# Performance work log

Measured on AMD Instinct MI355X. Metric: run time of the kernel, lower is better.

The kernel has to match this reference:

```python
import jax, jax.numpy as jnp
import numpy as np

# Mamba2 defaults (mamba_ssm): expand=2, headdim=64, d_conv=4, ngroups=1
D_MODEL, D_STATE, D_INNER, HEADDIM, D_CONV = 512, 64, 1024, 64, 4
NHEADS = D_INNER // HEADDIM  # 16
CONV_DIM = D_INNER + 2 * D_STATE  # 1152
D_IN_PROJ = 2 * D_INNER + 2 * D_STATE + NHEADS  # 2192
BATCH, SEQLEN = 2, 2048
RMS_EPS = 1.1920929e-07  # torch nn.RMSNorm eps=None -> fp32 machine eps
GNORM_EPS = 1e-5  # mamba_ssm RMSNormGated default


def _rms(t, w, eps):
    return t * jax.lax.rsqrt(jnp.mean(t * t, axis=-1, keepdims=True) + eps) * w


def _mamba2(u, in_w, conv_w, conv_b, dt_bias, A_log, Dp, gnorm_w, out_w):
    """Mamba2 block forward (ngroups=1). u: (b, l, d_model) -> (b, l, d_model)."""
    b, l, _ = u.shape
    zxbcdt = jnp.einsum('bld,ed->ble', u, in_w)  # (b, l, 2192)
    z = zxbcdt[..., :D_INNER]
    xBC = zxbcdt[..., D_INNER:D_INNER + CONV_DIM]
    dt = jax.nn.softplus(zxbcdt[..., -NHEADS:] + dt_bias)  # (b, l, h)
    # causal depthwise conv, kernel D_CONV, then SiLU
    xp = jnp.pad(xBC, ((0, 0), (D_CONV - 1, 0), (0, 0)))
    xBC = conv_b + sum(xp[:, i:i + l, :] * conv_w[:, i] for i in range(D_CONV))
    xBC = jax.nn.silu(xBC)
    x = xBC[..., :D_INNER].reshape(b, l, NHEADS, HEADDIM)
    Bm = xBC[..., D_INNER:D_INNER + D_STATE]  # (b, l, n)
    Cm = xBC[..., D_INNER + D_STATE:]         # (b, l, n)
    dA = jnp.exp(dt * (-jnp.exp(A_log)))      # (b, l, h), decay per head

    def step(h, inp):
        dA_t, dt_t, B_t, C_t, x_t = inp  # (b,h) (b,h) (b,n) (b,n) (b,h,p)
        h = h * dA_t[:, :, None, None] + jnp.einsum('bh,bhp,bn->bhpn', dt_t, x_t, B_t)
        y = jnp.einsum('bhpn,bn->bhp', h, C_t)
        return h, y

    h0 = jnp.zeros((b, NHEADS, HEADDIM, D_STATE), u.dtype)
    xs = (jnp.swapaxes(dA, 0, 1), jnp.swapaxes(dt, 0, 1), jnp.swapaxes(Bm, 0, 1),
          jnp.swapaxes(Cm, 0, 1), jnp.swapaxes(x, 0, 1))
    _, ys = jax.lax.scan(step, h0, xs)  # (l, b, h, p)
    y = jnp.swapaxes(ys, 0, 1) + x * Dp[None, None, :, None]
    y = y.reshape(b, l, D_INNER)
    # gated RMSNorm: norm(y * silu(z)) * weight
    y = y * jax.nn.silu(z)
    y = _rms(y, gnorm_w, GNORM_EPS)
    return jnp.einsum('bli,oi->blo', y, out_w)


def _layer(x, pos_emb, pixel_mask, norm_ssm_w, norm_ffn_w, ffn_w1, ffn_b1, ffn_w2, ffn_b2,
           f_in_w, f_conv_w, f_conv_b, f_dt_bias, f_A_log, f_D, f_gnorm_w, f_out_w,
           b_in_w, b_conv_w, b_conv_b, b_dt_bias, b_A_log, b_D, b_gnorm_w, b_out_w):
    si = _rms(x, norm_ssm_w, RMS_EPS) + pos_emb
    fwd = _mamba2(si, f_in_w, f_conv_w, f_conv_b, f_dt_bias, f_A_log, f_D, f_gnorm_w, f_out_w)
    bwd = jnp.flip(_mamba2(jnp.flip(si, 1), b_in_w, b_conv_w, b_conv_b, b_dt_bias,
                           b_A_log, b_D, b_gnorm_w, b_out_w), 1)
    ssm_out = (fwd + bwd) * pixel_mask[..., None]  # merge='add'
    x = x + ssm_out
    h = _rms(x, norm_ffn_w, RMS_EPS)
    h = jax.nn.gelu(h @ ffn_w1.T + ffn_b1, approximate=False)
    return x + (h @ ffn_w2.T + ffn_b2)


def setup_inputs() -> dict:
    key = jax.random.key(0)
    ks = jax.random.split(key, 16)
    f32 = jnp.float32
    inp = {}
    inp['x'] = jax.random.normal(ks[0], (BATCH, SEQLEN, D_MODEL), f32)
    inp['pos_emb'] = jax.random.normal(ks[1], (BATCH, SEQLEN, D_MODEL), f32) * 0.02
    inp['pixel_mask'] = jnp.ones((BATCH, SEQLEN), f32)
    inp['norm_ssm_w'] = jnp.ones((D_MODEL,), f32)
    inp['norm_ffn_w'] = jnp.ones((D_MODEL,), f32)
    d_ffn = 4 * D_MODEL
    inp['ffn_w1'] = jax.random.normal(ks[2], (d_ffn, D_MODEL), f32) * 0.02
    inp['ffn_b1'] = jnp.zeros((d_ffn,), f32)
    inp['ffn_w2'] = jax.random.normal(ks[3], (D_MODEL, d_ffn), f32) * 0.02
    inp['ffn_b2'] = jnp.zeros((D_MODEL,), f32)
    i = 4
    for pre in ('f', 'b'):
        inp[pre + '_in_w'] = jax.random.normal(ks[i], (D_IN_PROJ, D_MODEL), f32) * 0.02; i += 1
        inp[pre + '_conv_w'] = jax.random.uniform(ks[i], (CONV_DIM, D_CONV), f32, -0.5, 0.5); i += 1
        inp[pre + '_conv_b'] = jnp.zeros((CONV_DIM,), f32)
        dt0 = jnp.exp(jax.random.uniform(ks[i], (NHEADS,), f32) * (jnp.log(0.1) - jnp.log(0.001)) + jnp.log(0.001)); i += 1
        inp[pre + '_dt_bias'] = dt0 + jnp.log(-jnp.expm1(-dt0))  # inverse softplus
        inp[pre + '_A_log'] = jnp.log(jax.random.uniform(ks[i], (NHEADS,), f32, 1.0, 16.0)); i += 1
        inp[pre + '_D'] = jnp.ones((NHEADS,), f32)
        inp[pre + '_gnorm_w'] = jnp.ones((D_INNER,), f32)
        inp[pre + '_out_w'] = jax.random.normal(ks[i], (D_MODEL, D_INNER), f32) * 0.02; i += 1
    return inp


def reference(x, pos_emb, pixel_mask, norm_ssm_w, norm_ffn_w, ffn_w1, ffn_b1, ffn_w2, ffn_b2,
              f_in_w, f_conv_w, f_conv_b, f_dt_bias, f_A_log, f_D, f_gnorm_w, f_out_w,
              b_in_w, b_conv_w, b_conv_b, b_dt_bias, b_A_log, b_D, b_gnorm_w, b_out_w):
    return _layer(x, pos_emb, pixel_mask, norm_ssm_w, norm_ffn_w, ffn_w1, ffn_b1, ffn_w2, ffn_b2,
                  f_in_w, f_conv_w, f_conv_b, f_dt_bias, f_A_log, f_D, f_gnorm_w, f_out_w,
                  b_in_w, b_conv_w, b_conv_b, b_dt_bias, b_A_log, b_D, b_gnorm_w, b_out_w)
```

## Files before the change

kernel.cpp:

```cpp
#include <hip/hip_runtime.h>
#include <hip/hip_bf16.h>

typedef unsigned short u16;
typedef unsigned int u32;
typedef __bf16 bf16x8 __attribute__((ext_vector_type(8)));
typedef float f32x4 __attribute__((ext_vector_type(4)));

typedef __attribute__((address_space(1))) void gvoid_t;
typedef __attribute__((address_space(3))) void lvoid_t;
__device__ __forceinline__ void lds_cp16(void* lds, const void* g) {
    __builtin_amdgcn_global_load_lds((gvoid_t*)g, (lvoid_t*)lds, 16, 0, 0);
}

__device__ __forceinline__ float bf2f(u16 v) {
    u32 x = (u32)v << 16;
    return __builtin_bit_cast(float, x);
}
__device__ __forceinline__ u16 f2bf(float f) {
    return __builtin_bit_cast(u16, (__bf16)f);
}

__device__ __forceinline__ float wave_sum(float v) {
    #pragma unroll
    for (int o = 32; o > 0; o >>= 1) v += __shfl_xor(v, o);
    return v;
}

__device__ __forceinline__ void cvt4(const float* __restrict__ s, u16* __restrict__ d) {
    float4 v = *(const float4*)s;
    ushort4 o;
    o.x = f2bf(v.x); o.y = f2bf(v.y); o.z = f2bf(v.z); o.w = f2bf(v.w);
    *(ushort4*)d = o;
}

__global__ __launch_bounds__(256) void k_prep(
    const float* __restrict__ f_inw, const float* __restrict__ b_inw,
    const float* __restrict__ f_ow, const float* __restrict__ b_ow,
    const float* __restrict__ w1, const float* __restrict__ w2,
    u16* __restrict__ INWF, u16* __restrict__ INWB,
    u16* __restrict__ OWF, u16* __restrict__ OWB,
    u16* __restrict__ W1B, u16* __restrict__ W2B,
    const float* __restrict__ x, const float* __restrict__ pe,
    const float* __restrict__ wrms, u16* __restrict__ sib) {
    if (blockIdx.x < 5376) {
        int g = blockIdx.x * 256 + threadIdx.x;
        if (g < 294912) {
            int i = g * 4, n = i >> 9;
            if (n < 2192) cvt4(f_inw + i, INWF + i);
            else *(ushort4*)(INWF + i) = make_ushort4(0, 0, 0, 0);
            return;
        }
        g -= 294912;
        if (g < 294912) {
            int i = g * 4, n = i >> 9;
            if (n < 2192) cvt4(b_inw + i, INWB + i);
            else *(ushort4*)(INWB + i) = make_ushort4(0, 0, 0, 0);
            return;
        }
        g -= 294912;
        if (g < 131072) { cvt4(f_ow + g * 4, OWF + g * 4); return; }
        g -= 131072;
        if (g < 131072) { cvt4(b_ow + g * 4, OWB + g * 4); return; }
        g -= 131072;
        if (g < 262144) { cvt4(w1 + g * 4, W1B + g * 4); return; }
        g -= 262144;
        cvt4(w2 + g * 4, W2B + g * 4);
        return;
    }
    int row = (blockIdx.x - 5376) * 4 + (threadIdx.x >> 6);
    int lane = threadIdx.x & 63;
    size_t base = (size_t)row * 512 + lane * 4;
    float4 xa = *(const float4*)(x + base);
    float4 xb = *(const float4*)(x + base + 256);
    float ss = xa.x * xa.x + xa.y * xa.y + xa.z * xa.z + xa.w * xa.w
             + xb.x * xb.x + xb.y * xb.y + xb.z * xb.z + xb.w * xb.w;
    ss = wave_sum(ss);
    float sc = rsqrtf(ss * (1.f / 512.f) + 1.1920929e-07f);
    float4 pa = *(const float4*)(pe + base);
    float4 pb = *(const float4*)(pe + base + 256);
    float4 wa = *(const float4*)(wrms + lane * 4);
    float4 wb = *(const float4*)(wrms + lane * 4 + 256);
    ushort4 oa, obv;
    oa.x = f2bf(xa.x * sc * wa.x + pa.x);
    oa.y = f2bf(xa.y * sc * wa.y + pa.y);
    oa.z = f2bf(xa.z * sc * wa.z + pa.z);
    oa.w = f2bf(xa.w * sc * wa.w + pa.w);
    obv.x = f2bf(xb.x * sc * wb.x + pb.x);
    obv.y = f2bf(xb.y * sc * wb.y + pb.y);
    obv.z = f2bf(xb.z * sc * wb.z + pb.z);
    obv.w = f2bf(xb.w * sc * wb.w + pb.w);
    *(ushort4*)(sib + base) = oa;
    *(ushort4*)(sib + base + 256) = obv;
}

__global__ __launch_bounds__(256) void k_gemm_in(
    const u16* __restrict__ A, const u16* __restrict__ W0, const u16* __restrict__ W1,
    u16* __restrict__ Z0, u16* __restrict__ Z1,
    u16* __restrict__ XB0, u16* __restrict__ XB1) {
    const int z = blockIdx.z;
    const u16* W = z ? W1 : W0;
    u16* Z = z ? Z1 : Z0;
    u16* XB = z ? XB1 : XB0;
    const int K = 512;

    __shared__ __align__(16) u16 SMEM[24576];
    u16* As = SMEM;
    u16* Bs = SMEM + 12288;

    const int t = threadIdx.x;
    const int lane = t & 63;
    const int w = t >> 6;
    const int m0 = blockIdx.y * 128;
    const int n0 = blockIdx.x * 128;
    const int wm = (w >> 1) * 64;
    const int wn = (w & 1) * 64;
    const int fr = lane & 15;
    const int ksw = (((lane >> 4) ^ ((fr >> 1) & 3)) & 3) * 8;

    f32x4 acc[4][4];
    #pragma unroll
    for (int i = 0; i < 4; ++i)
        #pragma unroll
        for (int j = 0; j < 4; ++j) acc[i][j] = (f32x4){0.f, 0.f, 0.f, 0.f};

    auto STAGE = [&](int buf, int kt) {
        #pragma unroll
        for (int j = 0; j < 2; ++j) {
            int off16 = j * 256 + t;
            int row = off16 >> 2;
            int kc = (((off16 & 3) ^ ((row >> 1) & 3)) & 3) * 8;
            int gm = m0 + row;
            if (z) gm = (gm & ~2047) | (2047 - (gm & 2047));
            lds_cp16(As + buf * 4096 + off16 * 8, A + (size_t)gm * K + kt + kc);
            lds_cp16(Bs + buf * 4096 + off16 * 8, W + (size_t)(n0 + row) * K + kt + kc);
        }
    };

    const int NS = 16;
    STAGE(0, 0);
    STAGE(1, 32);
    asm volatile("s_waitcnt vmcnt(4)" ::: "memory");
    __builtin_amdgcn_s_barrier();
    __builtin_amdgcn_sched_barrier(0);
    int b0 = 0, b1 = 1, b2 = 2;
    for (int i = 0; i < NS; ++i) {
        if (i + 2 < NS) STAGE(b2, (i + 2) << 5);
        const u16* Ac = As + b0 * 4096;
        const u16* Bc = Bs + b0 * 4096;
        bf16x8 af[4], bfr[4];
        #pragma unroll
        for (int ii = 0; ii < 4; ++ii) af[ii] = *(const bf16x8*)(Ac + (wm + ii * 16 + fr) * 32 + ksw);
        #pragma unroll
        for (int ii = 0; ii < 4; ++ii) bfr[ii] = *(const bf16x8*)(Bc + (wn + ii * 16 + fr) * 32 + ksw);
        #pragma unroll
        for (int ii = 0; ii < 4; ++ii)
            #pragma unroll
            for (int jj = 0; jj < 4; ++jj)
                acc[ii][jj] = __builtin_amdgcn_mfma_f32_16x16x32_bf16(af[ii], bfr[jj], acc[ii][jj], 0, 0, 0);
        if (i + 1 < NS) {
            if (i + 2 < NS) asm volatile("s_waitcnt vmcnt(4) lgkmcnt(0)" ::: "memory");
            else            asm volatile("s_waitcnt vmcnt(0) lgkmcnt(0)" ::: "memory");
            __builtin_amdgcn_s_barrier();
            __builtin_amdgcn_sched_barrier(0);
        }
        int bt = b0; b0 = b1; b1 = b2; b2 = bt;
    }
    __syncthreads();
    const int PAD = 136;
    #pragma unroll
    for (int i = 0; i < 4; ++i) {
        int rloc = wm + i * 16 + (lane >> 4) * 4;
        #pragma unroll
        for (int j = 0; j < 4; ++j) {
            int cloc = wn + j * 16 + fr;
            #pragma unroll
            for (int r = 0; r < 4; ++r)
                SMEM[(rloc + r) * PAD + cloc] = f2bf(acc[i][j][r]);
        }
    }
    __syncthreads();
    if (n0 < 1024) {
        #pragma unroll
        for (int it = 0; it < 4; ++it) {
            int row = it * 32 + w * 8 + (lane >> 3);
            #pragma unroll
            for (int half = 0; half < 2; ++half) {
                int col = half * 64 + (lane & 7) * 8;
                uint4 v = *(const uint4*)(SMEM + row * PAD + col);
                *(uint4*)(Z + (size_t)(m0 + row) * 1024 + n0 + col) = v;
            }
        }
    } else {
        #pragma unroll
        for (int it = 0; it < 4; ++it) {
            int row = it * 32 + w * 8 + (lane >> 3);
            #pragma unroll
            for (int half = 0; half < 2; ++half) {
                int col = half * 64 + (lane & 7) * 8;
                int cx = n0 - 1024 + col;
                if (cx < 1168) {
                    uint4 v = *(const uint4*)(SMEM + row * PAD + col);
                    *(uint4*)(XB + (size_t)(m0 + row) * 1184 + cx) = v;
                }
            }
        }
    }
}

template <int EPI>
__global__ __launch_bounds__(256) void k_gemm128(
    const u16* __restrict__ A0, const u16* __restrict__ A1,
    const u16* __restrict__ W0, const u16* __restrict__ W1,
    u16* __restrict__ C0, u16* __restrict__ C1, int N, int K,
    const float* __restrict__ bias, const float* __restrict__ resid,
    float* __restrict__ outf) {
    const int z = blockIdx.z;
    const u16* A = z ? A1 : A0;
    const u16* W = z ? W1 : W0;
    u16* C = z ? C1 : C0;

    __shared__ __align__(16) u16 SMEM[24576];
    u16* As = SMEM;
    u16* Bs = SMEM + 12288;

    const int t = threadIdx.x;
    const int lane = t & 63;
    const int w = t >> 6;
    const int m0 = blockIdx.y * 128;
    const int n0 = blockIdx.x * 128;
    const int wm = (w >> 1) * 64;
    const int wn = (w & 1) * 64;
    const int fr = lane & 15;
    const int ksw = (((lane >> 4) ^ ((fr >> 1) & 3)) & 3) * 8;

    f32x4 acc[4][4];
    #pragma unroll
    for (int i = 0; i < 4; ++i)
        #pragma unroll
        for (int j = 0; j < 4; ++j) acc[i][j] = (f32x4){0.f, 0.f, 0.f, 0.f};

    auto STAGE = [&](int buf, int kt) {
        #pragma unroll
        for (int j = 0; j < 2; ++j) {
            int off16 = j * 256 + t;
            int row = off16 >> 2;
            int kc = (((off16 & 3) ^ ((row >> 1) & 3)) & 3) * 8;
            lds_cp16(As + buf * 4096 + off16 * 8, A + (size_t)(m0 + row) * K + kt + kc);
            lds_cp16(Bs + buf * 4096 + off16 * 8, W + (size_t)(n0 + row) * K + kt + kc);
        }
    };

    const int NS = K >> 5;
    STAGE(0, 0);
    STAGE(1, 32);
    asm volatile("s_waitcnt vmcnt(4)" ::: "memory");
    __builtin_amdgcn_s_barrier();
    __builtin_amdgcn_sched_barrier(0);
    int b0 = 0, b1 = 1, b2 = 2;
    for (int i = 0; i < NS; ++i) {
        if (i + 2 < NS) STAGE(b2, (i + 2) << 5);
        const u16* Ac = As + b0 * 4096;
        const u16* Bc = Bs + b0 * 4096;
        bf16x8 af[4], bfr[4];
        #pragma unroll
        for (int ii = 0; ii < 4; ++ii) af[ii] = *(const bf16x8*)(Ac + (wm + ii * 16 + fr) * 32 + ksw);
        #pragma unroll
        for (int ii = 0; ii < 4; ++ii) bfr[ii] = *(const bf16x8*)(Bc + (wn + ii * 16 + fr) * 32 + ksw);
        #pragma unroll
        for (int ii = 0; ii < 4; ++ii)
            #pragma unroll
            for (int jj = 0; jj < 4; ++jj)
                acc[ii][jj] = __builtin_amdgcn_mfma_f32_16x16x32_bf16(af[ii], bfr[jj], acc[ii][jj], 0, 0, 0);
        if (i + 1 < NS) {
            if (i + 2 < NS) asm volatile("s_waitcnt vmcnt(4) lgkmcnt(0)" ::: "memory");
            else            asm volatile("s_waitcnt vmcnt(0) lgkmcnt(0)" ::: "memory");
            __builtin_amdgcn_s_barrier();
            __builtin_amdgcn_sched_barrier(0);
        }
        int bt = b0; b0 = b1; b1 = b2; b2 = bt;
    }
    __syncthreads();
    const int PAD = 136;
    #pragma unroll
    for (int i = 0; i < 4; ++i) {
        int rloc = wm + i * 16 + (lane >> 4) * 4;
        #pragma unroll
        for (int j = 0; j < 4; ++j) {
            int cloc = wn + j * 16 + fr;
            float bv = (EPI == 1) ? bias[n0 + cloc] : 0.f;
            #pragma unroll
            for (int r = 0; r < 4; ++r) {
                float v = acc[i][j][r];
                if (EPI == 1) {
                    float xg = v + bv;
                    v = 0.5f * xg * (1.f + erff(xg * 0.70710678118654752f));
                }
                SMEM[(rloc + r) * PAD + cloc] = f2bf(v);
            }
        }
    }
    __syncthreads();
    #pragma unroll
    for (int it = 0; it < 4; ++it) {
        int row = it * 32 + w * 8 + (lane >> 3);
        #pragma unroll
        for (int half = 0; half < 2; ++half) {
            int col = half * 64 + (lane & 7) * 8;
            uint4 v = *(const uint4*)(SMEM + row * PAD + col);
            *(uint4*)(C + (size_t)(m0 + row) * N + n0 + col) = v;
        }
    }
}

template <int EPI>
__global__ __launch_bounds__(256) void k_gemm12864(
    const u16* __restrict__ A0, const u16* __restrict__ A1,
    const u16* __restrict__ W0, const u16* __restrict__ W1,
    u16* __restrict__ C0, u16* __restrict__ C1, int N, int K,
    const float* __restrict__ bias, const float* __restrict__ resid,
    float* __restrict__ outf) {
    const int z = blockIdx.z;
    const u16* A = z ? A1 : A0;
    const u16* W = z ? W1 : W0;
    u16* C = z ? C1 : C0;

    __shared__ __align__(16) u16 SMEM[18432];
    u16* As = SMEM;
    u16* Bs = SMEM + 12288;

    const int t = threadIdx.x;
    const int lane = t & 63;
    const int w = t >> 6;
    const int m0 = blockIdx.y * 128;
    const int n0 = blockIdx.x * 64;
    const int wm = w * 32;
    const int fr = lane & 15;
    const int ksw = (((lane >> 4) ^ ((fr >> 1) & 3)) & 3) * 8;

    f32x4 acc[2][4];
    #pragma unroll
    for (int i = 0; i < 2; ++i)
        #pragma unroll
        for (int j = 0; j < 4; ++j) acc[i][j] = (f32x4){0.f, 0.f, 0.f, 0.f};

    auto STAGE = [&](int buf, int kt) {
        #pragma unroll
        for (int j = 0; j < 2; ++j) {
            int off16 = j * 256 + t;
            int row = off16 >> 2;
            int kc = (((off16 & 3) ^ ((row >> 1) & 3)) & 3) * 8;
            lds_cp16(As + buf * 4096 + off16 * 8, A + (size_t)(m0 + row) * K + kt + kc);
        }
        int brow = t >> 2;
        int bkc = (((t & 3) ^ ((brow >> 1) & 3)) & 3) * 8;
        lds_cp16(Bs + buf * 2048 + t * 8, W + (size_t)(n0 + brow) * K + kt + bkc);
    };

    const int NS = K >> 5;
    STAGE(0, 0);
    STAGE(1, 32);
    asm volatile("s_waitcnt vmcnt(3)" ::: "memory");
    __builtin_amdgcn_s_barrier();
    __builtin_amdgcn_sched_barrier(0);
    int b0 = 0, b1 = 1, b2 = 2;
    for (int i = 0; i < NS; ++i) {
        if (i + 2 < NS) STAGE(b2, (i + 2) << 5);
        const u16* Ac = As + b0 * 4096;
        const u16* Bc = Bs + b0 * 2048;
        bf16x8 af[2], bfr[4];
        #pragma unroll
        for (int ii = 0; ii < 2; ++ii) af[ii] = *(const bf16x8*)(Ac + (wm + ii * 16 + fr) * 32 + ksw);
        #pragma unroll
        for (int jj = 0; jj < 4; ++jj) bfr[jj] = *(const bf16x8*)(Bc + (jj * 16 + fr) * 32 + ksw);
        #pragma unroll
        for (int ii = 0; ii < 2; ++ii)
            #pragma unroll
            for (int jj = 0; jj < 4; ++jj)
                acc[ii][jj] = __builtin_amdgcn_mfma_f32_16x16x32_bf16(af[ii], bfr[jj], acc[ii][jj], 0, 0, 0);
        if (i + 1 < NS) {
            if (i + 2 < NS) asm volatile("s_waitcnt vmcnt(3) lgkmcnt(0)" ::: "memory");
            else            asm volatile("s_waitcnt vmcnt(0) lgkmcnt(0)" ::: "memory");
            __builtin_amdgcn_s_barrier();
            __builtin_amdgcn_sched_barrier(0);
        }
        int bt = b0; b0 = b1; b1 = b2; b2 = bt;
    }
    __syncthreads();
    const int PAD = 72;
    #pragma unroll
    for (int i = 0; i < 2; ++i) {
        int rloc = wm + i * 16 + (lane >> 4) * 4;
        #pragma unroll
        for (int j = 0; j < 4; ++j) {
            int cloc = j * 16 + fr;
            float bv = (EPI == 1) ? bias[n0 + cloc] : 0.f;
            #pragma unroll
            for (int r = 0; r < 4; ++r) {
                float v = acc[i][j][r];
                if (EPI == 1) {
                    float xg = v + bv;
                    v = 0.5f * xg * (1.f + erff(xg * 0.70710678118654752f));
                }
                SMEM[(rloc + r) * PAD + cloc] = f2bf(v);
            }
        }
    }
    __syncthreads();
    #pragma unroll
    for (int it = 0; it < 4; ++it) {
        int row = it * 32 + w * 8 + (lane >> 3);
        int col = (lane & 7) * 8;
        uint4 v = *(const uint4*)(SMEM + row * PAD + col);
        *(uint4*)(C + (size_t)(m0 + row) * N + n0 + col) = v;
    }
}

template <int EPI>
__global__ __launch_bounds__(256) void k_gemm64(
    const u16* __restrict__ A0, const u16* __restrict__ A1,
    const u16* __restrict__ W0, const u16* __restrict__ W1,
    u16* __restrict__ C0, u16* __restrict__ C1, int N, int K,
    const float* __restrict__ bias, const float* __restrict__ resid,
    float* __restrict__ outf) {
    const int z = blockIdx.z;
    const u16* A = z ? A1 : A0;
    const u16* W = z ? W1 : W0;
    u16* C = z ? C1 : C0;

    __shared__ __align__(16) u16 SMEM[12288];
    u16* As = SMEM;
    u16* Bs = SMEM + 6144;

    const int t = threadIdx.x;
    const int lane = t & 63;
    const int w = t >> 6;
    const int m0 = blockIdx.y * 64;
    const int n0 = blockIdx.x * 64;
    const int wm = (w >> 1) * 32;
    const int wn = (w & 1) * 32;
    const int fr = lane & 15;
    const int ksw = (((lane >> 4) ^ ((fr >> 1) & 3)) & 3) * 8;

    f32x4 acc[2][2];
    #pragma unroll
    for (int i = 0; i < 2; ++i)
        #pragma unroll
        for (int j = 0; j < 2; ++j) acc[i][j] = (f32x4){0.f, 0.f, 0.f, 0.f};

    const int srow = t >> 2;
    const int skc = (((t & 3) ^ ((srow >> 1) & 3)) & 3) * 8;
    auto STAGE = [&](int buf, int kt) {
        lds_cp16(As + buf * 2048 + t * 8, A + (size_t)(m0 + srow) * K + kt + skc);
        lds_cp16(Bs + buf * 2048 + t * 8, W + (size_t)(n0 + srow) * K + kt + skc);
    };

    const int NS = K >> 5;
    STAGE(0, 0);
    STAGE(1, 32);
    asm volatile("s_waitcnt vmcnt(2)" ::: "memory");
    __builtin_amdgcn_s_barrier();
    __builtin_amdgcn_sched_barrier(0);
    int b0 = 0, b1 = 1, b2 = 2;
    for (int i = 0; i < NS; ++i) {
        if (i + 2 < NS) STAGE(b2, (i + 2) << 5);
        const u16* Ac = As + b0 * 2048;
        const u16* Bc = Bs + b0 * 2048;
        bf16x8 af[2], bfr[2];
        #pragma unroll
        for (int ii = 0; ii < 2; ++ii) af[ii] = *(const bf16x8*)(Ac + (wm + ii * 16 + fr) * 32 + ksw);
        #pragma unroll
        for (int jj = 0; jj < 2; ++jj) bfr[jj] = *(const bf16x8*)(Bc + (wn + jj * 16 + fr) * 32 + ksw);
        #pragma unroll
        for (int ii = 0; ii < 2; ++ii)
            #pragma unroll
            for (int jj = 0; jj < 2; ++jj)
                acc[ii][jj] = __builtin_amdgcn_mfma_f32_16x16x32_bf16(af[ii], bfr[jj], acc[ii][jj], 0, 0, 0);
        if (i + 1 < NS) {
            if (i + 2 < NS) asm volatile("s_waitcnt vmcnt(2) lgkmcnt(0)" ::: "memory");
            else            asm volatile("s_waitcnt vmcnt(0) lgkmcnt(0)" ::: "memory");
            __builtin_amdgcn_s_barrier();
            __builtin_amdgcn_sched_barrier(0);
        }
        int bt = b0; b0 = b1; b1 = b2; b2 = bt;
    }
    if (EPI == 2) {
        __syncthreads();
        float* EPF = (float*)SMEM;
        const int PADF = 68;
        #pragma unroll
        for (int i = 0; i < 2; ++i) {
            int rloc = wm + i * 16 + (lane >> 4) * 4;
            #pragma unroll
            for (int j = 0; j < 2; ++j) {
                int cloc = wn + j * 16 + fr;
                #pragma unroll
                for (int r = 0; r < 4; ++r)
                    EPF[(rloc + r) * PADF + cloc] = acc[i][j][r];
            }
        }
        __syncthreads();
        #pragma unroll
        for (int it = 0; it < 4; ++it) {
            int row = it * 16 + w * 4 + (lane >> 4);
            int col = (lane & 15) * 4;
            float4 v = *(const float4*)(EPF + row * PADF + col);
            int gcol = n0 + col;
            float4 bz = *(const float4*)(bias + gcol);
            float4 rv = *(const float4*)(resid + (size_t)(m0 + row) * N + gcol);
            float4 o;
            o.x = v.x + bz.x + rv.x;
            o.y = v.y + bz.y + rv.y;
            o.z = v.z + bz.z + rv.z;
            o.w = v.w + bz.w + rv.w;
            *(float4*)(outf + (size_t)(m0 + row) * N + gcol) = o;
        }
    } else {
        #pragma unroll
        for (int i = 0; i < 2; ++i) {
            int rbase = m0 + wm + i * 16 + (lane >> 4) * 4;
            #pragma unroll
            for (int j = 0; j < 2; ++j) {
                int col = n0 + wn + j * 16 + fr;
                #pragma unroll
                for (int r = 0; r < 4; ++r) {
                    int m = rbase + r;
                    float v = acc[i][j][r];
                    if (EPI == 0) {
                        C[(size_t)m * N + col] = f2bf(v);
                    } else {
                        float xg = v + bias[col];
                        C[(size_t)m * N + col] = f2bf(0.5f * xg * (1.f + erff(xg * 0.70710678118654752f)));
                    }
                }
            }
        }
    }
}

__global__ __launch_bounds__(160) void k_conv(
    const u16* __restrict__ xb0, const u16* __restrict__ xb1,
    const float* __restrict__ cw0, const float* __restrict__ cb0,
    const float* __restrict__ dtb0, const float* __restrict__ al0,
    const float* __restrict__ cw1, const float* __restrict__ cb1,
    const float* __restrict__ dtb1, const float* __restrict__ al1,
    u16* __restrict__ xc0, u16* __restrict__ xc1,
    float* __restrict__ dtO0, float* __restrict__ dAO0,
    float* __restrict__ dtO1, float* __restrict__ dAO1) {
    int g = blockIdx.x;
    int dir = g >> 9;
    int row0 = (g & 511) * 8;
    const u16* xb = dir ? xb1 : xb0;
    const float* cw = dir ? cw1 : cw0;
    const float* cb = dir ? cb1 : cb0;
    const float* dtb = dir ? dtb1 : dtb0;
    const float* al = dir ? al1 : al0;
    u16* xc = dir ? xc1 : xc0;
    float* dtO = dir ? dtO1 : dtO0;
    float* dAO = dir ? dAO1 : dAO0;
    int tl0 = row0 & 2047;
    int rbatch = row0 - tl0;
    int t = threadIdx.x;
    if (t < 144) {
        int col = t * 8;
        float cwa[8][4];
        #pragma unroll
        for (int j = 0; j < 8; ++j) {
            float4 c4 = *(const float4*)(cw + (col + j) * 4);
            cwa[j][0] = c4.x; cwa[j][1] = c4.y; cwa[j][2] = c4.z; cwa[j][3] = c4.w;
        }
        float cbv[8];
        float4 cb0v = *(const float4*)(cb + col);
        float4 cb1v = *(const float4*)(cb + col + 4);
        cbv[0] = cb0v.x; cbv[1] = cb0v.y; cbv[2] = cb0v.z; cbv[3] = cb0v.w;
        cbv[4] = cb1v.x; cbv[5] = cb1v.y; cbv[6] = cb1v.z; cbv[7] = cb1v.w;
        uint4 win[4];
        win[0] = win[1] = win[2] = make_uint4(0, 0, 0, 0);
        #pragma unroll
        for (int i = 0; i < 3; ++i) {
            int tt = tl0 - 3 + i;
            if (tt >= 0) win[i] = *(const uint4*)(xb + (size_t)(rbatch + tt) * 1184 + col);
        }
        for (int s = 0; s < 8; ++s) {
            win[3] = *(const uint4*)(xb + (size_t)(rbatch + tl0 + s) * 1184 + col);
            const u16* w0 = (const u16*)&win[0];
            const u16* w1 = (const u16*)&win[1];
            const u16* w2 = (const u16*)&win[2];
            const u16* w3 = (const u16*)&win[3];
            u16 ov[8];
            #pragma unroll
            for (int j = 0; j < 8; ++j) {
                float a = cbv[j] + bf2f(w0[j]) * cwa[j][0] + bf2f(w1[j]) * cwa[j][1]
                        + bf2f(w2[j]) * cwa[j][2] + bf2f(w3[j]) * cwa[j][3];
                ov[j] = f2bf(a / (1.f + expf(-a)));
            }
            *(uint4*)(xc + (size_t)(row0 + s) * 1152 + col) = *(const uint4*)ov;
            win[0] = win[1]; win[1] = win[2]; win[2] = win[3];
        }
    } else if (t < 160) {
        int hh = t - 144;
        float nal = -expf(al[hh]);
        float dtbv = dtb[hh];
        for (int s = 0; s < 8; ++s) {
            int row = row0 + s;
            float v = bf2f(xb[(size_t)row * 1184 + 1152 + hh]) + dtbv;
            float sp = (v > 20.f) ? v : log1pf(expf(v));
            dtO[row * 16 + hh] = sp;
            dAO[row * 16 + hh] = nal * sp;
        }
    }
}

__global__ __launch_bounds__(256) void k_ssd_state(
    const u16* __restrict__ xc0, const float* __restrict__ dt0, const float* __restrict__ ld0,
    const u16* __restrict__ xc1, const float* __restrict__ dt1, const float* __restrict__ ld1,
    float* __restrict__ S, float* __restrict__ Aprod) {
    int blk = blockIdx.x;
    int c = blk & 31, h = (blk >> 5) & 15, b = (blk >> 9) & 1, dir = blk >> 10;
    const u16* xc = dir ? xc1 : xc0;
    const float* dtp = dir ? dt1 : dt0;
    const float* ldp = dir ? ld1 : ld0;
    const int t = threadIdx.x, w = t >> 6, lane = t & 63;
    const int fr = lane & 15, fk = (lane >> 4) * 8;

    __shared__ __align__(16) u16 sBt[64 * 72];
    __shared__ __align__(16) u16 sXp[64 * 72];
    __shared__ float ssc[64];
    size_t row0 = (size_t)b * 2048 + c * 64;

    if (t < 64) {
        float v = ldp[(row0 + t) * 16 + h];
        float dtv = dtp[(row0 + t) * 16 + h];
        #pragma unroll
        for (int o = 1; o < 64; o <<= 1) {
            float u = __shfl_up(v, o);
            if (lane >= o) v += u;
        }
        float last = __shfl(v, 63);
        ssc[t] = dtv * expf(last - v);
        if (t == 63) Aprod[blk] = expf(v);
    }
    __syncthreads();
    #pragma unroll
    for (int i2 = t; i2 < 512; i2 += 256) {
        int r = i2 >> 3, e8 = (i2 & 7) * 8;
        size_t rb = (row0 + r) * 1152;
        uint4 bv = *(const uint4*)(xc + rb + 1024 + e8);
        uint4 xv = *(const uint4*)(xc + rb + h * 64 + e8);
        const u16* bs = (const u16*)&bv;
        const u16* xs = (const u16*)&xv;
        float sc = ssc[r];
        #pragma unroll
        for (int j = 0; j < 8; ++j) {
            sBt[(e8 + j) * 72 + r] = bs[j];
            sXp[(e8 + j) * 72 + r] = f2bf(bf2f(xs[j]) * sc);
        }
    }
    __syncthreads();

    f32x4 acc[4];
    #pragma unroll
    for (int j = 0; j < 4; ++j) acc[j] = (f32x4){0.f, 0.f, 0.f, 0.f};
    #pragma unroll
    for (int k0 = 0; k0 < 64; k0 += 32) {
        bf16x8 a = *(const bf16x8*)(sBt + (w * 16 + fr) * 72 + k0 + fk);
        #pragma unroll
        for (int j = 0; j < 4; ++j) {
            bf16x8 bb = *(const bf16x8*)(sXp + (j * 16 + fr) * 72 + k0 + fk);
            acc[j] = __builtin_amdgcn_mfma_f32_16x16x32_bf16(a, bb, acc[j], 0, 0, 0);
        }
    }
    float* Sb = S + (size_t)blk * 4096;
    int nb = w * 16 + (lane >> 4) * 4;
    #pragma unroll
    for (int j = 0; j < 4; ++j) {
        int p = j * 16 + fr;
        *(f32x4*)(Sb + p * 64 + nb) = acc[j];
    }
}

__global__ __launch_bounds__(256) void k_scan_carry(float* __restrict__ S,
                                                    const float* __restrict__ Aprod) {
    int g = blockIdx.x;
    int blk = g >> 4;
    int e = (g & 15) * 256 + threadIdx.x;
    size_t base = (size_t)blk * 32 * 4096 + e;
    float sv[32];
    #pragma unroll
    for (int c = 0; c < 32; ++c) sv[c] = S[base + (size_t)c * 4096];
    float ap[32];
    #pragma unroll
    for (int c = 0; c < 32; ++c) ap[c] = Aprod[blk * 32 + c];
    float h = 0.f;
    #pragma unroll
    for (int c = 0; c < 32; ++c) {
        S[base + (size_t)c * 4096] = h;
        h = ap[c] * h + sv[c];
    }
}

__global__ __launch_bounds__(256) void k_ssd_y(
    const u16* __restrict__ xc0, const float* __restrict__ dt0, const float* __restrict__ ld0,
    const float* __restrict__ Dv0, u16* __restrict__ y0,
    const u16* __restrict__ xc1, const float* __restrict__ dt1, const float* __restrict__ ld1,
    const float* __restrict__ Dv1, u16* __restrict__ y1,
    const float* __restrict__ S) {
    int blk = blockIdx.x;
    int c = blk & 31, h = (blk >> 5) & 15, b = (blk >> 9) & 1, dir = blk >> 10;
    const u16* xc = dir ? xc1 : xc0;
    const float* dtp = dir ? dt1 : dt0;
    const float* ldp = dir ? ld1 : ld0;
    u16* y = dir ? y1 : y0;
    const float Dh = (dir ? Dv1 : Dv0)[h];
    const int t = threadIdx.x, w = t >> 6, lane = t & 63;
    const int fr = lane & 15, fk = (lane >> 4) * 8;

    __shared__ __align__(16) u16 sB[64 * 72];
    __shared__ __align__(16) u16 sC[64 * 72];
    __shared__ __align__(16) u16 sXp[64 * 72];
    __shared__ __align__(16) u16 sHi[64 * 72];
    __shared__ __align__(16) u16 sLo[64 * 72];
    __shared__ float scl[64], sdt[64];
    size_t row0 = (size_t)b * 2048 + c * 64;

    if (t < 64) {
        float v = ldp[(row0 + t) * 16 + h];
        float dtv = dtp[(row0 + t) * 16 + h];
        #pragma unroll
        for (int o = 1; o < 64; o <<= 1) {
            float u = __shfl_up(v, o);
            if (lane >= o) v += u;
        }
        scl[t] = v;
        sdt[t] = dtv;
    }
    __syncthreads();
    #pragma unroll
    for (int i2 = t; i2 < 512; i2 += 256) {
        int r = i2 >> 3, e8 = (i2 & 7) * 8;
        size_t rb = (row0 + r) * 1152;
        *(uint4*)(sB + r * 72 + e8) = *(const uint4*)(xc + rb + 1024 + e8);
        *(uint4*)(sC + r * 72 + e8) = *(const uint4*)(xc + rb + 1088 + e8);
        uint4 xv = *(const uint4*)(xc + rb + h * 64 + e8);
        const u16* xs = (const u16*)&xv;
        float dtv = sdt[r];
        #pragma unroll
        for (int j = 0; j < 8; ++j) sXp[(e8 + j) * 72 + r] = f2bf(bf2f(xs[j]) * dtv);
    }
    #pragma unroll
    for (int i4 = t; i4 < 1024; i4 += 256) {
        int p = i4 >> 4, n4 = (i4 & 15) * 4;
        float4 hv = *(const float4*)(S + (size_t)blk * 4096 + p * 64 + n4);
        ushort4 hi4, lo4;
        hi4.x = f2bf(hv.x); lo4.x = f2bf(hv.x - bf2f(hi4.x));
        hi4.y = f2bf(hv.y); lo4.y = f2bf(hv.y - bf2f(hi4.y));
        hi4.z = f2bf(hv.z); lo4.z = f2bf(hv.z - bf2f(hi4.z));
        hi4.w = f2bf(hv.w); lo4.w = f2bf(hv.w - bf2f(hi4.w));
        *(ushort4*)(sHi + p * 72 + n4) = hi4;
        *(ushort4*)(sLo + p * 72 + n4) = lo4;
    }
    __syncthreads();

    f32x4 g[4], acc2[4];
    #pragma unroll
    for (int j = 0; j < 4; ++j) { g[j] = (f32x4){0.f,0.f,0.f,0.f}; acc2[j] = (f32x4){0.f,0.f,0.f,0.f}; }
    #pragma unroll
    for (int k0 = 0; k0 < 64; k0 += 32) {
        bf16x8 a = *(const bf16x8*)(sC + (w * 16 + fr) * 72 + k0 + fk);
        #pragma unroll
        for (int j = 0; j < 4; ++j) {
            bf16x8 bb = *(const bf16x8*)(sB + (j * 16 + fr) * 72 + k0 + fk);
            g[j] = __builtin_amdgcn_mfma_f32_16x16x32_bf16(a, bb, g[j], 0, 0, 0);
            bf16x8 bh = *(const bf16x8*)(sHi + (j * 16 + fr) * 72 + k0 + fk);
            acc2[j] = __builtin_amdgcn_mfma_f32_16x16x32_bf16(a, bh, acc2[j], 0, 0, 0);
            bf16x8 bl = *(const bf16x8*)(sLo + (j * 16 + fr) * 72 + k0 + fk);
            acc2[j] = __builtin_amdgcn_mfma_f32_16x16x32_bf16(a, bl, acc2[j], 0, 0, 0);
        }
    }
    __syncthreads();
    #pragma unroll
    for (int j = 0; j < 4; ++j) {
        int r = j * 16 + fr;
        #pragma unroll
        for (int reg = 0; reg < 4; ++reg) {
            int s = w * 16 + (lane >> 4) * 4 + reg;
            float val = (r <= s) ? expf(scl[s] - scl[r]) * g[j][reg] : 0.f;
            sC[s * 72 + r] = f2bf(val);
        }
    }
    __syncthreads();

    f32x4 acc1[4];
    #pragma unroll
    for (int j = 0; j < 4; ++j) acc1[j] = (f32x4){0.f, 0.f, 0.f, 0.f};
    #pragma unroll
    for (int k0 = 0; k0 < 64; k0 += 32) {
        bf16x8 a = *(const bf16x8*)(sC + (w * 16 + fr) * 72 + k0 + fk);
        #pragma unroll
        for (int j = 0; j < 4; ++j) {
            bf16x8 bb = *(const bf16x8*)(sXp + (j * 16 + fr) * 72 + k0 + fk);
            acc1[j] = __builtin_amdgcn_mfma_f32_16x16x32_bf16(a, bb, acc1[j], 0, 0, 0);
        }
    }
    #pragma unroll
    for (int reg = 0; reg < 4; ++reg) {
        int s = w * 16 + (lane >> 4) * 4 + reg;
        float es = expf(scl[s]);
        #pragma unroll
        for (int j = 0; j < 4; ++j) {
            int p = j * 16 + fr;
            float val = acc1[j][reg] + es * acc2[j][reg];
            u16 vh = f2bf(val);
            sB[s * 72 + p] = vh;
            sHi[s * 72 + p] = f2bf(val - bf2f(vh));
        }
    }
    __syncthreads();
    {
        int row = t >> 2;
        int cseg = (t & 3) * 16;
        size_t yrb = (row0 + row) * 1024 + h * 64 + cseg;
        size_t xrb = (row0 + row) * 1152 + h * 64 + cseg;
        #pragma unroll
        for (int u = 0; u < 2; ++u) {
            uint4 svh = *(const uint4*)(sB + row * 72 + cseg + u * 8);
            uint4 svl = *(const uint4*)(sHi + row * 72 + cseg + u * 8);
            uint4 xv = *(const uint4*)(xc + xrb + u * 8);
            const u16* ph = (const u16*)&svh;
            const u16* pl = (const u16*)&svl;
            const u16* px = (const u16*)&xv;
            u16 ov[8];
            #pragma unroll
            for (int e = 0; e < 8; ++e)
                ov[e] = f2bf(bf2f(ph[e]) + bf2f(pl[e]) + bf2f(px[e]) * Dh);
            *(uint4*)(y + yrb + u * 8) = *(const uint4*)ov;
        }
    }
}

__global__ __launch_bounds__(256) void k_gnorm(
    const u16* __restrict__ y0, const u16* __restrict__ z0,
    const float* __restrict__ gw0, u16* __restrict__ o0,
    const u16* __restrict__ y1, const u16* __restrict__ z1,
    const float* __restrict__ gw1, u16* __restrict__ o1) {
    int idx = blockIdx.x * 4 + (threadIdx.x >> 6);
    int dir = idx >> 12, row = idx & 4095;
    int lane = threadIdx.x & 63;
    const u16* y = dir ? y1 : y0;
    const u16* zp = dir ? z1 : z0;
    const float* gw = dir ? gw1 : gw0;
    u16* o = dir ? o1 : o0;
    size_t base = (size_t)row * 1024 + lane * 8;
    uint4 ya = *(const uint4*)(y + base);
    uint4 yb = *(const uint4*)(y + base + 512);
    uint4 za = *(const uint4*)(zp + base);
    uint4 zb = *(const uint4*)(zp + base + 512);
    const u16* yap = (const u16*)&ya;
    const u16* ybp = (const u16*)&yb;
    const u16* zap = (const u16*)&za;
    const u16* zbp = (const u16*)&zb;
    float v[16];
    float ss = 0.f;
    #pragma unroll
    for (int j = 0; j < 8; ++j) {
        float zf = bf2f(zap[j]);
        v[j] = bf2f(yap[j]) * (zf / (1.f + expf(-zf)));
        ss += v[j] * v[j];
    }
    #pragma unroll
    for (int j = 0; j < 8; ++j) {
        float zf = bf2f(zbp[j]);
        v[8 + j] = bf2f(ybp[j]) * (zf / (1.f + expf(-zf)));
        ss += v[8 + j] * v[8 + j];
    }
    ss = wave_sum(ss);
    float sc = rsqrtf(ss * (1.f / 1024.f) + 1e-5f);
    float4 g0 = *(const float4*)(gw + lane * 8);
    float4 g1 = *(const float4*)(gw + lane * 8 + 4);
    float4 g2 = *(const float4*)(gw + 512 + lane * 8);
    float4 g3 = *(const float4*)(gw + 512 + lane * 8 + 4);
    const float* gp0 = (const float*)&g0;
    const float* gp1 = (const float*)&g1;
    const float* gp2 = (const float*)&g2;
    const float* gp3 = (const float*)&g3;
    u16 oa[8], obv[8];
    #pragma unroll
    for (int j = 0; j < 4; ++j) {
        oa[j] = f2bf(v[j] * sc * gp0[j]);
        oa[4 + j] = f2bf(v[4 + j] * sc * gp1[j]);
        obv[j] = f2bf(v[8 + j] * sc * gp2[j]);
        obv[4 + j] = f2bf(v[12 + j] * sc * gp3[j]);
    }
    *(uint4*)(o + base) = *(const uint4*)oa;
    *(uint4*)(o + base + 512) = *(const uint4*)obv;
}

__global__ __launch_bounds__(256) void k_add_rms(
    const float* __restrict__ x, const u16* __restrict__ of,
    const u16* __restrict__ ob, const float* __restrict__ mask,
    const float* __restrict__ wrms,
    float* __restrict__ x2, u16* __restrict__ o) {
    int row = blockIdx.x * 4 + (threadIdx.x >> 6);
    int lane = threadIdx.x & 63;
    int bb = row >> 11, tl = row & 2047;
    size_t fb = (size_t)((bb << 11) + (2047 - tl)) * 512;
    float m = mask[row];
    size_t base = (size_t)row * 512 + lane * 4;
    size_t fo = fb + lane * 4;
    float4 xa = *(const float4*)(x + base);
    float4 xb = *(const float4*)(x + base + 256);
    ushort4 fa = *(const ushort4*)(of + base);
    ushort4 fbv = *(const ushort4*)(of + base + 256);
    ushort4 ba = *(const ushort4*)(ob + fo);
    ushort4 bbv = *(const ushort4*)(ob + fo + 256);
    float va[4], vb[4];
    va[0] = xa.x + (bf2f(fa.x) + bf2f(ba.x)) * m;
    va[1] = xa.y + (bf2f(fa.y) + bf2f(ba.y)) * m;
    va[2] = xa.z + (bf2f(fa.z) + bf2f(ba.z)) * m;
    va[3] = xa.w + (bf2f(fa.w) + bf2f(ba.w)) * m;
    vb[0] = xb.x + (bf2f(fbv.x) + bf2f(bbv.x)) * m;
    vb[1] = xb.y + (bf2f(fbv.y) + bf2f(bbv.y)) * m;
    vb[2] = xb.z + (bf2f(fbv.z) + bf2f(bbv.z)) * m;
    vb[3] = xb.w + (bf2f(fbv.w) + bf2f(bbv.w)) * m;
    *(float4*)(x2 + base) = (float4){va[0], va[1], va[2], va[3]};
    *(float4*)(x2 + base + 256) = (float4){vb[0], vb[1], vb[2], vb[3]};
    float ss = va[0]*va[0] + va[1]*va[1] + va[2]*va[2] + va[3]*va[3]
             + vb[0]*vb[0] + vb[1]*vb[1] + vb[2]*vb[2] + vb[3]*vb[3];
    ss = wave_sum(ss);
    float sc = rsqrtf(ss * (1.f / 512.f) + 1.1920929e-07f);
    float4 wa = *(const float4*)(wrms + lane * 4);
    float4 wb = *(const float4*)(wrms + lane * 4 + 256);
    ushort4 oa, obv;
    oa.x = f2bf(va[0] * sc * wa.x);
    oa.y = f2bf(va[1] * sc * wa.y);
    oa.z = f2bf(va[2] * sc * wa.z);
    oa.w = f2bf(va[3] * sc * wa.w);
    obv.x = f2bf(vb[0] * sc * wb.x);
    obv.y = f2bf(vb[1] * sc * wb.y);
    obv.z = f2bf(vb[2] * sc * wb.z);
    obv.w = f2bf(vb[3] * sc * wb.w);
    *(ushort4*)(o + base) = oa;
    *(ushort4*)(o + base + 256) = obv;
}

extern "C" void kernel_launch(void* const* d_in, const int* in_sizes, int n_in,
                              void* d_out, int out_size, void* d_ws, size_t ws_size,
                              hipStream_t stream) {
    const float* x = (const float*)d_in[0];
    const float* pe = (const float*)d_in[1];
    const float* mask = (const float*)d_in[2];
    const float* nsw = (const float*)d_in[3];
    const float* nfw = (const float*)d_in[4];
    const float* w1 = (const float*)d_in[5];
    const float* b1 = (const float*)d_in[6];
    const float* w2 = (const float*)d_in[7];
    const float* b2 = (const float*)d_in[8];
    const float* f_inw = (const float*)d_in[9];
    const float* f_cw = (const float*)d_in[10];
    const float* f_cb = (const float*)d_in[11];
    const float* f_dtb = (const float*)d_in[12];
    const float* f_al = (const float*)d_in[13];
    const float* f_D = (const float*)d_in[14];
    const float* f_gw = (const float*)d_in[15];
    const float* f_ow = (const float*)d_in[16];
    const float* b_inw = (const float*)d_in[17];
    const float* b_cw = (const float*)d_in[18];
    const float* b_cb = (const float*)d_in[19];
    const float* b_dtb = (const float*)d_in[20];
    const float* b_al = (const float*)d_in[21];
    const float* b_D = (const float*)d_in[22];
    const float* b_gw = (const float*)d_in[23];
    const float* b_ow = (const float*)d_in[24];
    float* out = (float*)d_out;

    char* ws = (char*)d_ws;
    u16* Z0   = (u16*)(ws + 0);
    u16* Z1   = (u16*)(ws + 8388608);
    u16* XB0  = (u16*)(ws + 16777216);
    u16* XB1  = (u16*)(ws + 26476544);
    u16* INWF = (u16*)(ws + 36175872);
    u16* INWB = (u16*)(ws + 38535168);
    u16* SIB  = (u16*)(ws + 40894464);
    u16* XC0  = (u16*)(ws + 36175872);
    u16* XC1  = (u16*)(ws + 45613056);
    float* dtF = (float*)(ws + 55050240);
    float* dAF = (float*)(ws + 55312384);
    float* dtB = (float*)(ws + 55574528);
    float* dAB = (float*)(ws + 55836672);
    u16* Y0   = (u16*)(ws + 16777216);
    u16* Y1   = (u16*)(ws + 25165824);
    u16* YG0  = (u16*)(ws + 36175872);
    u16* YG1  = (u16*)(ws + 44564480);
    u16* OP0  = (u16*)(ws + 0);
    u16* OP1  = (u16*)(ws + 4194304);
    float* X2 = (float*)(ws + 8388608);
    u16* X2B  = (u16*)(ws + 0);
    u16* HACT = (u16*)(ws + 16777216);
    u16* OWF = (u16*)(ws + 56098816);
    u16* OWB = (u16*)(ws + 57147392);
    u16* W1B = (u16*)(ws + 58195968);
    u16* W2B = (u16*)(ws + 60293120);
    float* SBUF = (float*)(ws + 62390272);
    float* APR  = (float*)(ws + 95944704);

    k_prep<<<6400, 256, 0, stream>>>(f_inw, b_inw, f_ow, b_ow, w1, w2,
                                     INWF, INWB, OWF, OWB, W1B, W2B,
                                     x, pe, nsw, SIB);
    k_gemm_in<<<dim3(18, 32, 2), 256, 0, stream>>>(SIB, INWF, INWB, Z0, Z1, XB0, XB1);
    k_conv<<<1024, 160, 0, stream>>>(XB0, XB1, f_cw, f_cb, f_dtb, f_al,
                                     b_cw, b_cb, b_dtb, b_al,
                                     XC0, XC1, dtF, dAF, dtB, dAB);
    k_ssd_state<<<2048, 256, 0, stream>>>(XC0, dtF, dAF, XC1, dtB, dAB, SBUF, APR);
    k_scan_carry<<<1024, 256, 0, stream>>>(SBUF, APR);
    k_ssd_y<<<2048, 256, 0, stream>>>(XC0, dtF, dAF, f_D, Y0,
                                      XC1, dtB, dAB, b_D, Y1, SBUF);
    k_gnorm<<<2048, 256, 0, stream>>>(Y0, Z0, f_gw, YG0, Y1, Z1, b_gw, YG1);
    k_gemm12864<0><<<dim3(8, 32, 2), 256, 0, stream>>>(YG0, YG1, OWF, OWB, OP0, OP1, 512, 1024,
                                                       nullptr, nullptr, nullptr);
    k_add_rms<<<1024, 256, 0, stream>>>(x, OP0, OP1, mask, nfw, X2, X2B);
    k_gemm128<1><<<dim3(16, 32, 1), 256, 0, stream>>>(X2B, X2B, W1B, W1B, HACT, HACT, 2048, 512,
                                                      b1, nullptr, nullptr);
    k_gemm64<2><<<dim3(8, 64, 1), 256, 0, stream>>>(HACT, HACT, W2B, W2B, nullptr, nullptr,
                                                    512, 2048, b2, X2, out);
}
```

Baseline: 305.9 us.

## Swizzle GEMM workgroup order, pack LDS transposes, reuse hi buffer for lo state

All four GEMM kernels remap the flat workgroup index with a stride-8 swizzle so that consecutively launched blocks cover a spread of output tiles, aiming to place neighbouring tiles on different XCDs and improve L2 locality. The chunk-state and chunk-output kernels now stage two rows per thread and write packed 32-bit pairs into the transposed LDS tiles, halving the number of narrow LDS stores. The output kernel also drops the separate sLo buffer: it keeps the fp32 state in registers, runs the hi pass, then overwrites sHi with the lo residual and runs a second MFMA pass. This lowers LDS footprint, which may raise occupancy, at the cost of two extra barriers and more live registers.

```diff
diff --git a/kernel.cpp b/kernel.cpp
--- a/kernel.cpp
+++ b/kernel.cpp
@@ -110,8 +110,11 @@
     const int t = threadIdx.x;
     const int lane = t & 63;
     const int w = t >> 6;
-    const int m0 = blockIdx.y * 128;
-    const int n0 = blockIdx.x * 128;
+    const int nwg = gridDim.x * gridDim.y;
+    const int wg = blockIdx.y * gridDim.x + blockIdx.x;
+    const int swz = (wg & 7) * (nwg >> 3) + (wg >> 3);
+    const int m0 = (swz / gridDim.x) * 128;
+    const int n0 = (swz % gridDim.x) * 128;
     const int wm = (w >> 1) * 64;
     const int wn = (w & 1) * 64;
     const int fr = lane & 15;
@@ -226,8 +229,11 @@
     const int t = threadIdx.x;
     const int lane = t & 63;
     const int w = t >> 6;
-    const int m0 = blockIdx.y * 128;
-    const int n0 = blockIdx.x * 128;
+    const int nwg = gridDim.x * gridDim.y;
+    const int wg = blockIdx.y * gridDim.x + blockIdx.x;
+    const int swz = (wg & 7) * (nwg >> 3) + (wg >> 3);
+    const int m0 = (swz / gridDim.x) * 128;
+    const int n0 = (swz % gridDim.x) * 128;
     const int wm = (w >> 1) * 64;
     const int wn = (w & 1) * 64;
     const int fr = lane & 15;
@@ -331,8 +337,11 @@
     const int t = threadIdx.x;
     const int lane = t & 63;
     const int w = t >> 6;
-    const int m0 = blockIdx.y * 128;
-    const int n0 = blockIdx.x * 64;
+    const int nwg = gridDim.x * gridDim.y;
+    const int wg = blockIdx.y * gridDim.x + blockIdx.x;
+    const int swz = (wg & 7) * (nwg >> 3) + (wg >> 3);
+    const int m0 = (swz / gridDim.x) * 128;
+    const int n0 = (swz % gridDim.x) * 64;
     const int wm = w * 32;
     const int fr = lane & 15;
     const int ksw = (((lane >> 4) ^ ((fr >> 1) & 3)) & 3) * 8;
@@ -434,8 +443,11 @@
     const int t = threadIdx.x;
     const int lane = t & 63;
     const int w = t >> 6;
-    const int m0 = blockIdx.y * 64;
-    const int n0 = blockIdx.x * 64;
+    const int nwg = gridDim.x * gridDim.y;
+    const int wg = blockIdx.y * gridDim.x + blockIdx.x;
+    const int swz = (wg & 7) * (nwg >> 3) + (wg >> 3);
+    const int m0 = (swz / gridDim.x) * 64;
+    const int n0 = (swz % gridDim.x) * 64;
     const int wm = (w >> 1) * 32;
     const int wn = (w & 1) * 32;
     const int fr = lane & 15;
@@ -640,19 +652,25 @@
         if (t == 63) Aprod[blk] = expf(v);
     }
     __syncthreads();
-    #pragma unroll
-    for (int i2 = t; i2 < 512; i2 += 256) {
-        int r = i2 >> 3, e8 = (i2 & 7) * 8;
-        size_t rb = (row0 + r) * 1152;
-        uint4 bv = *(const uint4*)(xc + rb + 1024 + e8);
-        uint4 xv = *(const uint4*)(xc + rb + h * 64 + e8);
-        const u16* bs = (const u16*)&bv;
-        const u16* xs = (const u16*)&xv;
-        float sc = ssc[r];
+    {
+        int rp = (t >> 3) * 2;
+        int e8 = (t & 7) * 8;
+        size_t rb0 = (row0 + rp) * 1152;
+        size_t rb1 = (row0 + rp + 1) * 1152;
+        uint4 bv0 = *(const uint4*)(xc + rb0 + 1024 + e8);
+        uint4 bv1 = *(const uint4*)(xc + rb1 + 1024 + e8);
+        uint4 xv0 = *(const uint4*)(xc + rb0 + h * 64 + e8);
+        uint4 xv1 = *(const uint4*)(xc + rb1 + h * 64 + e8);
+        const u16* pb0 = (const u16*)&bv0;
+        const u16* pb1 = (const u16*)&bv1;
+        const u16* px0 = (const u16*)&xv0;
+        const u16* px1 = (const u16*)&xv1;
+        float s0 = ssc[rp], s1 = ssc[rp + 1];
         #pragma unroll
         for (int j = 0; j < 8; ++j) {
-            sBt[(e8 + j) * 72 + r] = bs[j];
-            sXp[(e8 + j) * 72 + r] = f2bf(bf2f(xs[j]) * sc);
+            *(u32*)(sBt + (e8 + j) * 72 + rp) = (u32)pb0[j] | ((u32)pb1[j] << 16);
+            u32 xw = (u32)f2bf(bf2f(px0[j]) * s0) | ((u32)f2bf(bf2f(px1[j]) * s1) << 16);
+            *(u32*)(sXp + (e8 + j) * 72 + rp) = xw;
         }
     }
     __syncthreads();
@@ -718,7 +736,6 @@
     __shared__ __align__(16) u16 sC[64 * 72];
     __shared__ __align__(16) u16 sXp[64 * 72];
     __shared__ __align__(16) u16 sHi[64 * 72];
-    __shared__ __align__(16) u16 sLo[64 * 72];
     __shared__ float scl[64], sdt[64];
     size_t row0 = (size_t)b * 2048 + c * 64;
 
@@ -734,29 +751,38 @@
         sdt[t] = dtv;
     }
     __syncthreads();
-    #pragma unroll
-    for (int i2 = t; i2 < 512; i2 += 256) {
-        int r = i2 >> 3, e8 = (i2 & 7) * 8;
-        size_t rb = (row0 + r) * 1152;
-        *(uint4*)(sB + r * 72 + e8) = *(const uint4*)(xc + rb + 1024 + e8);
-        *(uint4*)(sC + r * 72 + e8) = *(const uint4*)(xc + rb + 1088 + e8);
-        uint4 xv = *(const uint4*)(xc + rb + h * 64 + e8);
-        const u16* xs = (const u16*)&xv;
-        float dtv = sdt[r];
-        #pragma unroll
-        for (int j = 0; j < 8; ++j) sXp[(e8 + j) * 72 + r] = f2bf(bf2f(xs[j]) * dtv);
-    }
-    #pragma unroll
-    for (int i4 = t; i4 < 1024; i4 += 256) {
+    {
+        int rp = (t >> 3) * 2;
+        int e8 = (t & 7) * 8;
+        size_t rb0 = (row0 + rp) * 1152;
+        size_t rb1 = (row0 + rp + 1) * 1152;
+        *(uint4*)(sB + rp * 72 + e8)       = *(const uint4*)(xc + rb0 + 1024 + e8);
+        *(uint4*)(sB + (rp + 1) * 72 + e8) = *(const uint4*)(xc + rb1 + 1024 + e8);
+        *(uint4*)(sC + rp * 72 + e8)       = *(const uint4*)(xc + rb0 + 1088 + e8);
+        *(uint4*)(sC + (rp + 1) * 72 + e8) = *(const uint4*)(xc + rb1 + 1088 + e8);
+        uint4 xv0 = *(const uint4*)(xc + rb0 + h * 64 + e8);
+        uint4 xv1 = *(const uint4*)(xc + rb1 + h * 64 + e8);
+        const u16* px0 = (const u16*)&xv0;
+        const u16* px1 = (const u16*)&xv1;
+        float d0 = sdt[rp], d1 = sdt[rp + 1];
+        #pragma unroll
+        for (int j = 0; j < 8; ++j) {
+            u32 xw = (u32)f2bf(bf2f(px0[j]) * d0) | ((u32)f2bf(bf2f(px1[j]) * d1) << 16);
+            *(u32*)(sXp + (e8 + j) * 72 + rp) = xw;
+        }
+    }
+    float4 hvr[4];
+    #pragma unroll
+    for (int q = 0; q < 4; ++q) {
+        int i4 = t + q * 256;
         int p = i4 >> 4, n4 = (i4 & 15) * 4;
-        float4 hv = *(const float4*)(S + (size_t)blk * 4096 + p * 64 + n4);
-        ushort4 hi4, lo4;
-        hi4.x = f2bf(hv.x); lo4.x = f2bf(hv.x - bf2f(hi4.x));
-        hi4.y = f2bf(hv.y); lo4.y = f2bf(hv.y - bf2f(hi4.y));
-        hi4.z = f2bf(hv.z); lo4.z = f2bf(hv.z - bf2f(hi4.z));
-        hi4.w = f2bf(hv.w); lo4.w = f2bf(hv.w - bf2f(hi4.w));
+        hvr[q] = *(const float4*)(S + (size_t)blk * 4096 + p * 64 + n4);
+        ushort4 hi4;
+        hi4.x = f2bf(hvr[q].x);
+        hi4.y = f2bf(hvr[q].y);
+        hi4.z = f2bf(hvr[q].z);
+        hi4.w = f2bf(hvr[q].w);
         *(ushort4*)(sHi + p * 72 + n4) = hi4;
-        *(ushort4*)(sLo + p * 72 + n4) = lo4;
     }
     __syncthreads();
 
@@ -772,7 +798,27 @@
             g[j] = __builtin_amdgcn_mfma_f32_16x16x32_bf16(a, bb, g[j], 0, 0, 0);
             bf16x8 bh = *(const bf16x8*)(sHi + (j * 16 + fr) * 72 + k0 + fk);
             acc2[j] = __builtin_amdgcn_mfma_f32_16x16x32_bf16(a, bh, acc2[j], 0, 0, 0);
-            bf16x8 bl = *(const bf16x8*)(sLo + (j * 16 + fr) * 72 + k0 + fk);
+        }
+    }
+    __syncthreads();
+    #pragma unroll
+    for (int q = 0; q < 4; ++q) {
+        int i4 = t + q * 256;
+        int p = i4 >> 4, n4 = (i4 & 15) * 4;
+        ushort4 lo4;
+        lo4.x = f2bf(hvr[q].x - bf2f(f2bf(hvr[q].x)));
+        lo4.y = f2bf(hvr[q].y - bf2f(f2bf(hvr[q].y)));
+        lo4.z = f2bf(hvr[q].z - bf2f(f2bf(hvr[q].z)));
+        lo4.w = f2bf(hvr[q].w - bf2f(f2bf(hvr[q].w)));
+        *(ushort4*)(sHi + p * 72 + n4) = lo4;
+    }
+    __syncthreads();
+    #pragma unroll
+    for (int k0 = 0; k0 < 64; k0 += 32) {
+        bf16x8 a = *(const bf16x8*)(sC + (w * 16 + fr) * 72 + k0 + fk);
+        #pragma unroll
+        for (int j = 0; j < 4; ++j) {
+            bf16x8 bl = *(const bf16x8*)(sHi + (j * 16 + fr) * 72 + k0 + fk);
             acc2[j] = __builtin_amdgcn_mfma_f32_16x16x32_bf16(a, bl, acc2[j], 0, 0, 0);
         }
     }
```

Result: faster. 290.5 us, median of 2 (-5.1%).
